# Kernel tuning notes

Measured on AMD Instinct MI355X. Metric: run time of the kernel, lower is better.

## Reference

```python
import jax, jax.numpy as jnp
import numpy as np

NEG_SLOPE = 0.2
N_NODES = 50000
N_EDGES = 800000
NUM_GRAPHS = 128
IN_F, HID_F, OUT_F = 64, 64, 64


def _gat_layer(x, src, dst, W, a_src, a_dst, b, n_nodes):
    # x: [N, Fin] -> out: [N, Fout]; single-head PyG GATConv with self-loops
    xp = x @ W                                   # [N, Fout]
    alpha_src = xp @ a_src                       # [N]
    alpha_dst = xp @ a_dst                       # [N]
    e = jax.nn.leaky_relu(alpha_src[src] + alpha_dst[dst], NEG_SLOPE)  # [E]
    # segment softmax over incoming edges of each dst node
    m = jax.ops.segment_max(e, dst, num_segments=n_nodes)
    ex = jnp.exp(e - m[dst])
    denom = jax.ops.segment_sum(ex, dst, num_segments=n_nodes)
    alpha = ex / denom[dst]                      # [E]
    out = jax.ops.segment_sum(alpha[:, None] * xp[src], dst, num_segments=n_nodes)
    return out + b


def setup_inputs() -> dict:
    key = jax.random.key(0)
    ks = jax.random.split(key, 12)
    x = jax.random.normal(ks[0], (N_NODES, IN_F), dtype=jnp.float32)
    edge_index = jax.random.randint(ks[1], (2, N_EDGES), 0, N_NODES, dtype=jnp.int64 if jax.config.jax_enable_x64 else jnp.int32)
    batch = jnp.sort(jax.random.randint(ks[2], (N_NODES,), 0, NUM_GRAPHS, dtype=edge_index.dtype))
    s = 0.1
    W1 = jax.random.normal(ks[3], (IN_F, HID_F), dtype=jnp.float32) * s
    att_src1 = jax.random.normal(ks[4], (HID_F,), dtype=jnp.float32) * s
    att_dst1 = jax.random.normal(ks[5], (HID_F,), dtype=jnp.float32) * s
    b1 = jax.random.normal(ks[6], (HID_F,), dtype=jnp.float32) * s
    W2 = jax.random.normal(ks[7], (HID_F, OUT_F), dtype=jnp.float32) * s
    att_src2 = jax.random.normal(ks[8], (OUT_F,), dtype=jnp.float32) * s
    att_dst2 = jax.random.normal(ks[9], (OUT_F,), dtype=jnp.float32) * s
    b2 = jax.random.normal(ks[10], (OUT_F,), dtype=jnp.float32) * s
    return {"x": x, "edge_index": edge_index, "batch": batch,
            "W1": W1, "att_src1": att_src1, "att_dst1": att_dst1, "b1": b1,
            "W2": W2, "att_src2": att_src2, "att_dst2": att_dst2, "b2": b2}


def reference(x, edge_index, batch, W1, att_src1, att_dst1, b1, W2, att_src2, att_dst2, b2):
    n = x.shape[0]
    # add self-loops (PyG GATConv default)
    loops = jnp.arange(n, dtype=edge_index.dtype)
    src = jnp.concatenate([edge_index[0], loops])
    dst = jnp.concatenate([edge_index[1], loops])
    h = _gat_layer(x, src, dst, W1, att_src1, att_dst1, b1, n)
    h = jax.nn.relu(h)  # dropout = identity at eval
    h = _gat_layer(h, src, dst, W2, att_src2, att_dst2, b2, n)
    h = jax.nn.relu(h)
    # scatter_mean over graphs
    sums = jax.ops.segment_sum(h, batch, num_segments=NUM_GRAPHS)
    counts = jax.ops.segment_sum(jnp.ones((n,), dtype=h.dtype), batch, num_segments=NUM_GRAPHS)
    return sums / jnp.maximum(counts, 1.0)[:, None]
```

## Files before the change

kernel.cpp:

```cpp
#include <hip/hip_runtime.h>
#include <hip/hip_fp16.h>

#define FEAT 64
#define BK   64
#define CAP  1536
#define MAXB 1024
#define SEPT 16
#define CHUNK (256 * SEPT)
#define LG   4

typedef _Float16 f16;
typedef __attribute__((ext_vector_type(8))) _Float16 f16x8;
typedef __attribute__((ext_vector_type(4))) float    f32x4;

struct GemmSm {
    union {
        struct { f16 Xs[64][72]; f16 Wt[64][72]; };
        float Cs[4][16][68];
    };
    float asl[64], adl[64];
};

__device__ __forceinline__ void gemm_tile(
    GemmSm& sm, int row0, const float* __restrict__ xin,
    const float* __restrict__ W, const float* __restrict__ avs,
    const float* __restrict__ avd, unsigned* __restrict__ xph,
    float* __restrict__ as_, float* __restrict__ ad_, int n)
{
    const int t = threadIdx.x;
    const int lane = t & 63;
    const int wave = t >> 6;

    if (t < 64) sm.asl[t] = avs[t];
    else if (t < 128) sm.adl[t - 64] = avd[t - 64];

    for (int i = t; i < 64 * 16; i += 256) {
        const int r = i >> 4, c4 = (i & 15) << 2;
        const int gr = row0 + r;
        float4 v = make_float4(0.f, 0.f, 0.f, 0.f);
        if (gr < n) v = *(const float4*)(xin + (size_t)gr * FEAT + c4);
        sm.Xs[r][c4 + 0] = (f16)v.x; sm.Xs[r][c4 + 1] = (f16)v.y;
        sm.Xs[r][c4 + 2] = (f16)v.z; sm.Xs[r][c4 + 3] = (f16)v.w;
    }
    for (int i = t; i < 64 * 16; i += 256) {
        const int k = i >> 4, c4 = (i & 15) << 2;
        const float4 v = *(const float4*)(W + k * FEAT + c4);
        sm.Wt[c4 + 0][k] = (f16)v.x; sm.Wt[c4 + 1][k] = (f16)v.y;
        sm.Wt[c4 + 2][k] = (f16)v.z; sm.Wt[c4 + 3][k] = (f16)v.w;
    }
    __syncthreads();

    const int mrow = (wave << 4) + (lane & 15);
    const int kg = lane >> 4;
    const f16x8 a0 = *(const f16x8*)(&sm.Xs[mrow][kg * 8]);
    const f16x8 a1 = *(const f16x8*)(&sm.Xs[mrow][32 + kg * 8]);

    f32x4 acc[4];
#pragma unroll
    for (int nt = 0; nt < 4; ++nt) {
        const int ncol = nt * 16 + (lane & 15);
        const f16x8 b0 = *(const f16x8*)(&sm.Wt[ncol][kg * 8]);
        const f16x8 b1 = *(const f16x8*)(&sm.Wt[ncol][32 + kg * 8]);
        f32x4 c = {0.f, 0.f, 0.f, 0.f};
        c = __builtin_amdgcn_mfma_f32_16x16x32_f16(a0, b0, c, 0, 0, 0);
        c = __builtin_amdgcn_mfma_f32_16x16x32_f16(a1, b1, c, 0, 0, 0);
        acc[nt] = c;
    }
    __syncthreads();

#pragma unroll
    for (int nt = 0; nt < 4; ++nt)
#pragma unroll
        for (int reg = 0; reg < 4; ++reg)
            sm.Cs[wave][(lane >> 4) * 4 + reg][nt * 16 + (lane & 15)] = acc[nt][reg];

    for (int i = lane; i < 16 * 32; i += 64) {
        const int r = i >> 5, fp = i & 31;
        const int node = row0 + (wave << 4) + r;
        if (node < n) {
            const __half2 pk = __floats2half2_rn(sm.Cs[wave][r][2 * fp],
                                                 sm.Cs[wave][r][2 * fp + 1]);
            xph[(size_t)node * 32 + fp] = *(const unsigned*)&pk;
        }
    }
    {
        const int r = lane >> 2, q = lane & 3;
        float s1 = 0.f, s2 = 0.f;
#pragma unroll
        for (int j = 0; j < 16; ++j) {
            const int c = q * 16 + j;
            const float v = sm.Cs[wave][r][c];
            s1 += v * sm.asl[c];
            s2 += v * sm.adl[c];
        }
        s1 += __shfl_xor(s1, 1); s1 += __shfl_xor(s1, 2);
        s2 += __shfl_xor(s2, 1); s2 += __shfl_xor(s2, 2);
        const int node = row0 + (wave << 4) + r;
        if (q == 0 && node < n) { as_[node] = s1; ad_[node] = s2; }
    }
}

__global__ __launch_bounds__(256) void scatter_gemm1_kernel(
    const int* __restrict__ src, const int* __restrict__ dst,
    int* __restrict__ bcur, unsigned* __restrict__ ebuf,
    const float* __restrict__ x, const float* __restrict__ W,
    const float* __restrict__ a_src, const float* __restrict__ a_dst,
    unsigned* __restrict__ xph, float* __restrict__ as_, float* __restrict__ ad_,
    int n, int E, int nbuck, int nchunks)
{
    __shared__ union {
        struct {
            unsigned staged[CHUNK];
            int hist[MAXB]; int lofs[MAXB]; int base[MAXB];
        } s;
        GemmSm g;
    } sm;

    const int t = threadIdx.x;
    const int lane = t & 63;
    const int wave = t >> 6;

    if (blockIdx.x < (unsigned)nchunks) {
        for (int i = t; i < nbuck; i += 256) sm.s.hist[i] = 0;
        __syncthreads();

        const int e0 = blockIdx.x * CHUNK;
        const int total = min(E - e0, CHUNK);

        unsigned code[SEPT]; int bk[SEPT], rk[SEPT];
#pragma unroll
        for (int k = 0; k < SEPT; ++k) {
            const int e = e0 + t + k * 256;
            bk[k] = -1;
            if (e < E) {
                const int s_ = src[e], d = dst[e];
                bk[k] = d >> 6;
                code[k] = ((unsigned)s_ << 6) | (unsigned)(d & 63);
                rk[k] = atomicAdd(&sm.s.hist[bk[k]], 1);
            }
        }
        __syncthreads();

        if (wave == 0) {
            int carry = 0;
            for (int b0 = 0; b0 < nbuck; b0 += 64) {
                const int idx = b0 + lane;
                int v = (idx < nbuck) ? sm.s.hist[idx] : 0;
                const int orig = v;
#pragma unroll
                for (int o = 1; o < 64; o <<= 1) {
                    const int u = __shfl_up(v, o);
                    if (lane >= o) v += u;
                }
                if (idx < nbuck) sm.s.lofs[idx] = v - orig + carry;
                carry += __shfl(v, 63);
            }
        }
        __syncthreads();
        for (int i = t; i < nbuck; i += 256) {
            const int hv = sm.s.hist[i];
            sm.s.base[i] = hv ? atomicAdd(&bcur[i], hv) : 0;
        }
        __syncthreads();

#pragma unroll
        for (int k = 0; k < SEPT; ++k) {
            if (bk[k] >= 0)
                sm.s.staged[sm.s.lofs[bk[k]] + rk[k]] =
                    ((unsigned)bk[k] << 22) | code[k];
        }
        __syncthreads();

        for (int i = t; i < total; i += 256) {
            const unsigned e = sm.s.staged[i];
            const int bkt = e >> 22;
            const int pos = sm.s.base[bkt] + (i - sm.s.lofs[bkt]);
            if (pos < CAP) ebuf[(size_t)bkt * CAP + pos] = e & 0x3FFFFFu;
        }
    } else {
        gemm_tile(sm.g, (blockIdx.x - nchunks) * 64, x, W, a_src, a_dst,
                  xph, as_, ad_, n);
    }
}

__device__ __forceinline__ void agg_phaseB_to(
    const unsigned* scode, const float* sw, const int* startsL,
    const float* adb, const float* __restrict__ as_,
    const uint4* __restrict__ xph4, const float* __restrict__ bias,
    float* __restrict__ hout, int hstride, int g0, int n)
{
    const int lane = threadIdx.x & 63;
    const int wave = threadIdx.x >> 6;
    const int np = lane >> 5;
    const int q  = (lane >> 3) & 3;
    const int fo = lane & 7;

    for (int pair = wave; pair < BK / 2; pair += 8) {
        const int node = pair * 2 + np;
        const int g = g0 + node;
        const int gc = (g < n) ? g : (n - 1);
        const int st = startsL[node], en = startsL[node + 1];

        float a[8] = {0.f, 0.f, 0.f, 0.f, 0.f, 0.f, 0.f, 0.f};
        float wsum = 0.f;

        int i = st + q;
        for (; i + 12 < en; i += 16) {
            const unsigned c0 = scode[i];
            const unsigned c1 = scode[i + 4];
            const unsigned c2 = scode[i + 8];
            const unsigned c3 = scode[i + 12];
            const float w0 = sw[i], w1 = sw[i + 4], w2 = sw[i + 8], w3 = sw[i + 12];
            const uint4 x0 = xph4[(size_t)(c0 >> 6) * 8 + fo];
            const uint4 x1 = xph4[(size_t)(c1 >> 6) * 8 + fo];
            const uint4 x2 = xph4[(size_t)(c2 >> 6) * 8 + fo];
            const uint4 x3 = xph4[(size_t)(c3 >> 6) * 8 + fo];
#pragma unroll
            for (int u = 0; u < 4; ++u) {
                const uint4 xv = (u == 0) ? x0 : (u == 1) ? x1 : (u == 2) ? x2 : x3;
                const float wv = (u == 0) ? w0 : (u == 1) ? w1 : (u == 2) ? w2 : w3;
                const __half2 p0 = *(const __half2*)&xv.x;
                const __half2 p1 = *(const __half2*)&xv.y;
                const __half2 p2 = *(const __half2*)&xv.z;
                const __half2 p3 = *(const __half2*)&xv.w;
                a[0] += wv * __low2float(p0);  a[1] += wv * __high2float(p0);
                a[2] += wv * __low2float(p1);  a[3] += wv * __high2float(p1);
                a[4] += wv * __low2float(p2);  a[5] += wv * __high2float(p2);
                a[6] += wv * __low2float(p3);  a[7] += wv * __high2float(p3);
            }
            wsum += (w0 + w1) + (w2 + w3);
        }
        for (; i < en; i += 4) {
            const unsigned c0 = scode[i];
            const float w0 = sw[i];
            const uint4 xv = xph4[(size_t)(c0 >> 6) * 8 + fo];
            const __half2 p0 = *(const __half2*)&xv.x;
            const __half2 p1 = *(const __half2*)&xv.y;
            const __half2 p2 = *(const __half2*)&xv.z;
            const __half2 p3 = *(const __half2*)&xv.w;
            a[0] += w0 * __low2float(p0);  a[1] += w0 * __high2float(p0);
            a[2] += w0 * __low2float(p1);  a[3] += w0 * __high2float(p1);
            a[4] += w0 * __low2float(p2);  a[5] += w0 * __high2float(p2);
            a[6] += w0 * __low2float(p3);  a[7] += w0 * __high2float(p3);
            wsum += w0;
        }

#pragma unroll
        for (int j = 0; j < 8; ++j) {
            a[j] += __shfl_xor(a[j], 8);
            a[j] += __shfl_xor(a[j], 16);
        }
        wsum += __shfl_xor(wsum, 8);
        wsum += __shfl_xor(wsum, 16);

        float tt = as_[gc] + adb[node];
        tt = (tt >= 0.f) ? tt : 0.2f * tt;
        const float wself = __expf(tt);
        const uint4 xg = xph4[(size_t)gc * 8 + fo];
        const __half2 s0 = *(const __half2*)&xg.x;
        const __half2 s1 = *(const __half2*)&xg.y;
        const __half2 s2 = *(const __half2*)&xg.z;
        const __half2 s3 = *(const __half2*)&xg.w;
        const float dinv = 1.f / (wsum + wself);
        const float4 bA = *(const float4*)(bias + 8 * fo);
        const float4 bB = *(const float4*)(bias + 8 * fo + 4);

        if (q == 0 && g < n) {
            float4 vA, vB;
            vA.x = fmaxf((a[0] + wself * __low2float(s0))  * dinv + bA.x, 0.f);
            vA.y = fmaxf((a[1] + wself * __high2float(s0)) * dinv + bA.y, 0.f);
            vA.z = fmaxf((a[2] + wself * __low2float(s1))  * dinv + bA.z, 0.f);
            vA.w = fmaxf((a[3] + wself * __high2float(s1)) * dinv + bA.w, 0.f);
            vB.x = fmaxf((a[4] + wself * __low2float(s2))  * dinv + bB.x, 0.f);
            vB.y = fmaxf((a[5] + wself * __high2float(s2)) * dinv + bB.y, 0.f);
            vB.z = fmaxf((a[6] + wself * __low2float(s3))  * dinv + bB.z, 0.f);
            vB.w = fmaxf((a[7] + wself * __high2float(s3)) * dinv + bB.w, 0.f);
            *(float4*)(hout + (size_t)node * hstride + 8 * fo)     = vA;
            *(float4*)(hout + (size_t)node * hstride + 8 * fo + 4) = vB;
        }
    }
}

__global__ __launch_bounds__(512) void sortagg1_gemm2_kernel(
    const int* __restrict__ bcur, unsigned* __restrict__ ebuf,
    int* __restrict__ startsG,
    const float* __restrict__ asA, const float* __restrict__ adA,
    const uint4* __restrict__ xphA, const float* __restrict__ b1,
    const float* __restrict__ W2, const float* __restrict__ asrc2,
    const float* __restrict__ adst2,
    unsigned* __restrict__ xphB, float* __restrict__ asB, float* __restrict__ adB,
    int n)
{
    __shared__ float htile[64][68];
    __shared__ union {
        struct { unsigned scode[CAP]; float sw[CAP]; int hist[BK]; int cur[BK]; } a;
        GemmSm g;
    } sm;
    __shared__ int starts[BK + 1];
    __shared__ float adb[BK];

    const int b = blockIdx.x;
    const int t = threadIdx.x;
    const int lane = t & 63, wave = t >> 6;
    const int g0 = b * BK;
    const int row0 = g0;

    if (t < BK) {
        sm.a.hist[t] = 0;
        adb[t] = (g0 + t < n) ? adA[g0 + t] : 0.f;
    }
    __syncthreads();

    int cnt = bcur[b];
    if (cnt > CAP) cnt = CAP;
    unsigned* eb = ebuf + (size_t)b * CAP;

    unsigned c[3];
#pragma unroll
    for (int k = 0; k < 3; ++k) {
        const int i = t + k * 512;
        if (i < cnt) { c[k] = eb[i]; atomicAdd(&sm.a.hist[c[k] & 63], 1); }
    }
    __syncthreads();
    if (wave == 0) {
        int v = sm.a.hist[lane];
#pragma unroll
        for (int o = 1; o < 64; o <<= 1) {
            const int u = __shfl_up(v, o);
            if (lane >= o) v += u;
        }
        starts[lane + 1] = v;
        sm.a.cur[lane] = v - sm.a.hist[lane];
        if (lane == 0) starts[0] = 0;
    }
    __syncthreads();
#pragma unroll
    for (int k = 0; k < 3; ++k) {
        const int i = t + k * 512;
        if (i < cnt) { const int p = atomicAdd(&sm.a.cur[c[k] & 63], 1); sm.a.scode[p] = c[k]; }
    }
    __syncthreads();

    unsigned cc[3]; float vv[3];
#pragma unroll
    for (int k = 0; k < 3; ++k) {
        const int i = t + k * 512;
        if (i < cnt) { cc[k] = sm.a.scode[i]; eb[i] = cc[k]; vv[k] = asA[cc[k] >> 6]; }
    }
    if (t <= BK) startsG[b * (BK + 1) + t] = starts[t];
#pragma unroll
    for (int k = 0; k < 3; ++k) {
        const int i = t + k * 512;
        if (i < cnt) {
            float tt = vv[k] + adb[cc[k] & 63];
            tt = (tt >= 0.f) ? tt : 0.2f * tt;
            sm.a.sw[i] = __expf(tt);
        }
    }
    __syncthreads();

    agg_phaseB_to(sm.a.scode, sm.a.sw, starts, adb, asA, xphA, b1,
                  &htile[0][0], 68, g0, n);
    __syncthreads();

    if (t < 64) sm.g.asl[t] = asrc2[t];
    else if (t < 128) sm.g.adl[t - 64] = adst2[t - 64];

    for (int i = t; i < 64 * 16; i += 512) {
        const int r = i >> 4, c4 = (i & 15) << 2;
        const float4 v = *(const float4*)(&htile[r][c4]);
        sm.g.Xs[r][c4 + 0] = (f16)v.x; sm.g.Xs[r][c4 + 1] = (f16)v.y;
        sm.g.Xs[r][c4 + 2] = (f16)v.z; sm.g.Xs[r][c4 + 3] = (f16)v.w;
    }
    for (int i = t; i < 64 * 16; i += 512) {
        const int k = i >> 4, c4 = (i & 15) << 2;
        const float4 v = *(const float4*)(W2 + k * FEAT + c4);
        sm.g.Wt[c4 + 0][k] = (f16)v.x; sm.g.Wt[c4 + 1][k] = (f16)v.y;
        sm.g.Wt[c4 + 2][k] = (f16)v.z; sm.g.Wt[c4 + 3][k] = (f16)v.w;
    }
    __syncthreads();

    f32x4 acc[4];
    if (wave < 4) {
        const int mrow = (wave << 4) + (lane & 15);
        const int kg = lane >> 4;
        const f16x8 a0 = *(const f16x8*)(&sm.g.Xs[mrow][kg * 8]);
        const f16x8 a1 = *(const f16x8*)(&sm.g.Xs[mrow][32 + kg * 8]);
#pragma unroll
        for (int nt = 0; nt < 4; ++nt) {
            const int ncol = nt * 16 + (lane & 15);
            const f16x8 b0 = *(const f16x8*)(&sm.g.Wt[ncol][kg * 8]);
            const f16x8 b1v = *(const f16x8*)(&sm.g.Wt[ncol][32 + kg * 8]);
            f32x4 cacc = {0.f, 0.f, 0.f, 0.f};
            cacc = __builtin_amdgcn_mfma_f32_16x16x32_f16(a0, b0, cacc, 0, 0, 0);
            cacc = __builtin_amdgcn_mfma_f32_16x16x32_f16(a1, b1v, cacc, 0, 0, 0);
            acc[nt] = cacc;
        }
    }
    __syncthreads();
    if (wave < 4) {
#pragma unroll
        for (int nt = 0; nt < 4; ++nt)
#pragma unroll
            for (int reg = 0; reg < 4; ++reg)
                sm.g.Cs[wave][(lane >> 4) * 4 + reg][nt * 16 + (lane & 15)] = acc[nt][reg];
    }
    __syncthreads();

    for (int i = t; i < 64 * 32; i += 512) {
        const int r = i >> 5, fp = i & 31;
        const int node = row0 + r;
        if (node < n) {
            const __half2 pk = __floats2half2_rn(sm.g.Cs[r >> 4][r & 15][2 * fp],
                                                 sm.g.Cs[r >> 4][r & 15][2 * fp + 1]);
            xphB[(size_t)node * 32 + fp] = *(const unsigned*)&pk;
        }
    }
    if (t < 256) {
        const int r = t >> 2, q = t & 3;
        float s1 = 0.f, s2 = 0.f;
#pragma unroll
        for (int j = 0; j < 16; ++j) {
            const int cidx = q * 16 + j;
            const float v = sm.g.Cs[r >> 4][r & 15][cidx];
            s1 += v * sm.g.asl[cidx];
            s2 += v * sm.g.adl[cidx];
        }
        s1 += __shfl_xor(s1, 1); s1 += __shfl_xor(s1, 2);
        s2 += __shfl_xor(s2, 1); s2 += __shfl_xor(s2, 2);
        const int node = row0 + r;
        if (q == 0 && node < n) { asB[node] = s1; adB[node] = s2; }
    }
}

__global__ __launch_bounds__(512) void agg2_pool_kernel(
    const unsigned* __restrict__ ebuf, const int* __restrict__ startsG,
    const float* __restrict__ as_, const float* __restrict__ ad_,
    const uint4* __restrict__ xph4, const float* __restrict__ bias,
    const int* __restrict__ batch, float* __restrict__ gpart,
    float* __restrict__ osum, int n)
{
    __shared__ unsigned scode[CAP];
    __shared__ float    sw[CAP];
    __shared__ int startsL[BK + 1];
    __shared__ float adb[BK];
    __shared__ int batchL[BK];
    __shared__ float gpartW[8][2][LG][FEAT];

    const int b = blockIdx.x;
    const int t = threadIdx.x;
    const int lane = t & 63, wave = t >> 6;
    const int g0 = b * BK;

    if (t < BK) {
        const int g = g0 + t;
        adb[t] = (g < n) ? ad_[g] : 0.f;
        batchL[t] = batch[(g < n) ? g : (n - 1)];
    }
    if (t <= BK) startsL[t] = startsG[b * (BK + 1) + t];
    for (int i = t; i < 8 * 2 * LG * FEAT; i += 512) ((float*)gpartW)[i] = 0.f;
    __syncthreads();

    const int cnt = startsL[BK];
    const unsigned* eb = ebuf + (size_t)b * CAP;

    unsigned cc[3]; float vv[3];
#pragma unroll
    for (int k = 0; k < 3; ++k) {
        const int i = t + k * 512;
        if (i < cnt) { cc[k] = eb[i]; vv[k] = as_[cc[k] >> 6]; }
    }
#pragma unroll
    for (int k = 0; k < 3; ++k) {
        const int i = t + k * 512;
        if (i < cnt) {
            float tt = vv[k] + adb[cc[k] & 63];
            tt = (tt >= 0.f) ? tt : 0.2f * tt;
            scode[i] = cc[k]; sw[i] = __expf(tt);
        }
    }
    __syncthreads();

    const int np = lane >> 5;
    const int q  = (lane >> 3) & 3;
    const int fo = lane & 7;
    const int gbase = batchL[0];

    for (int pair = wave; pair < BK / 2; pair += 8) {
        const int node = pair * 2 + np;
        const int g = g0 + node;
        const int gc = (g < n) ? g : (n - 1);
        const int st = startsL[node], en = startsL[node + 1];

        float a[8] = {0.f, 0.f, 0.f, 0.f, 0.f, 0.f, 0.f, 0.f};
        float wsum = 0.f;

        int i = st + q;
        for (; i + 12 < en; i += 16) {
            const unsigned c0 = scode[i];
            const unsigned c1 = scode[i + 4];
            const unsigned c2 = scode[i + 8];
            const unsigned c3 = scode[i + 12];
            const float w0 = sw[i], w1 = sw[i + 4], w2 = sw[i + 8], w3 = sw[i + 12];
            const uint4 x0 = xph4[(size_t)(c0 >> 6) * 8 + fo];
            const uint4 x1 = xph4[(size_t)(c1 >> 6) * 8 + fo];
            const uint4 x2 = xph4[(size_t)(c2 >> 6) * 8 + fo];
            const uint4 x3 = xph4[(size_t)(c3 >> 6) * 8 + fo];
#pragma unroll
            for (int u = 0; u < 4; ++u) {
                const uint4 xv = (u == 0) ? x0 : (u == 1) ? x1 : (u == 2) ? x2 : x3;
                const float wv = (u == 0) ? w0 : (u == 1) ? w1 : (u == 2) ? w2 : w3;
                const __half2 p0 = *(const __half2*)&xv.x;
                const __half2 p1 = *(const __half2*)&xv.y;
                const __half2 p2 = *(const __half2*)&xv.z;
                const __half2 p3 = *(const __half2*)&xv.w;
                a[0] += wv * __low2float(p0);  a[1] += wv * __high2float(p0);
                a[2] += wv * __low2float(p1);  a[3] += wv * __high2float(p1);
                a[4] += wv * __low2float(p2);  a[5] += wv * __high2float(p2);
                a[6] += wv * __low2float(p3);  a[7] += wv * __high2float(p3);
            }
            wsum += (w0 + w1) + (w2 + w3);
        }
        for (; i < en; i += 4) {
            const unsigned c0 = scode[i];
            const float w0 = sw[i];
            const uint4 xv = xph4[(size_t)(c0 >> 6) * 8 + fo];
            const __half2 p0 = *(const __half2*)&xv.x;
            const __half2 p1 = *(const __half2*)&xv.y;
            const __half2 p2 = *(const __half2*)&xv.z;
            const __half2 p3 = *(const __half2*)&xv.w;
            a[0] += w0 * __low2float(p0);  a[1] += w0 * __high2float(p0);
            a[2] += w0 * __low2float(p1);  a[3] += w0 * __high2float(p1);
            a[4] += w0 * __low2float(p2);  a[5] += w0 * __high2float(p2);
            a[6] += w0 * __low2float(p3);  a[7] += w0 * __high2float(p3);
            wsum += w0;
        }

#pragma unroll
        for (int j = 0; j < 8; ++j) {
            a[j] += __shfl_xor(a[j], 8);
            a[j] += __shfl_xor(a[j], 16);
        }
        wsum += __shfl_xor(wsum, 8);
        wsum += __shfl_xor(wsum, 16);

        float tt = as_[gc] + adb[node];
        tt = (tt >= 0.f) ? tt : 0.2f * tt;
        const float wself = __expf(tt);
        const uint4 xg = xph4[(size_t)gc * 8 + fo];
        const __half2 s0 = *(const __half2*)&xg.x;
        const __half2 s1 = *(const __half2*)&xg.y;
        const __half2 s2 = *(const __half2*)&xg.z;
        const __half2 s3 = *(const __half2*)&xg.w;
        const float dinv = 1.f / (wsum + wself);
        const float4 bA = *(const float4*)(bias + 8 * fo);
        const float4 bB = *(const float4*)(bias + 8 * fo + 4);

        if (q == 0 && g < n) {
            float4 vA, vB;
            vA.x = fmaxf((a[0] + wself * __low2float(s0))  * dinv + bA.x, 0.f);
            vA.y = fmaxf((a[1] + wself * __high2float(s0)) * dinv + bA.y, 0.f);
            vA.z = fmaxf((a[2] + wself * __low2float(s1))  * dinv + bA.z, 0.f);
            vA.w = fmaxf((a[3] + wself * __high2float(s1)) * dinv + bA.w, 0.f);
            vB.x = fmaxf((a[4] + wself * __low2float(s2))  * dinv + bB.x, 0.f);
            vB.y = fmaxf((a[5] + wself * __high2float(s2)) * dinv + bB.y, 0.f);
            vB.z = fmaxf((a[6] + wself * __low2float(s3))  * dinv + bB.z, 0.f);
            vB.w = fmaxf((a[7] + wself * __high2float(s3)) * dinv + bB.w, 0.f);

            const int lg = batchL[node] - gbase;
            if (lg < LG) {
                float* p = &gpartW[wave][np][lg][8 * fo];
                float4 oA = *(float4*)p;
                float4 oB = *(float4*)(p + 4);
                oA.x += vA.x; oA.y += vA.y; oA.z += vA.z; oA.w += vA.w;
                oB.x += vB.x; oB.y += vB.y; oB.z += vB.z; oB.w += vB.w;
                *(float4*)p = oA;
                *(float4*)(p + 4) = oB;
            } else {
                float* o = osum + (size_t)batchL[node] * FEAT + 8 * fo;
                atomicAdd(o + 0, vA.x); atomicAdd(o + 1, vA.y);
                atomicAdd(o + 2, vA.z); atomicAdd(o + 3, vA.w);
                atomicAdd(o + 4, vB.x); atomicAdd(o + 5, vB.y);
                atomicAdd(o + 6, vB.z); atomicAdd(o + 7, vB.w);
            }
        }
    }
    __syncthreads();

    if (t < LG * FEAT) {
        const int lg = t >> 6, f = t & 63;
        float s = 0.f;
#pragma unroll
        for (int w = 0; w < 8; ++w)
            s += gpartW[w][0][lg][f] + gpartW[w][1][lg][f];
        gpart[((size_t)b * LG + lg) * FEAT + f] = s;
    }
}

__device__ __forceinline__ int lower_bound_i(const int* a, int n, int key)
{
    int lo = 0, hi = n;
    while (lo < hi) {
        const int mid = (lo + hi) >> 1;
        if (a[mid] < key) lo = mid + 1; else hi = mid;
    }
    return lo;
}

__global__ __launch_bounds__(64) void pool_reduce_kernel(
    const float* __restrict__ gpart, const float* __restrict__ osum,
    const int* __restrict__ batch, float* __restrict__ out, int n, int G)
{
    const int g = blockIdx.x;
    const int lane = threadIdx.x;

    const int lo = lower_bound_i(batch, n, g);
    const int hi = lower_bound_i(batch, n, g + 1);

    float s = osum[(size_t)g * FEAT + lane];
    if (lo < hi) {
        const int b0 = lo >> 6, b1 = (hi - 1) >> 6;
        for (int b = b0; b <= b1; ++b) {
            const int base = batch[b << 6];
            const int lg = g - base;
            if (lg >= 0 && lg < LG)
                s += gpart[((size_t)b * LG + lg) * FEAT + lane];
        }
    }
    out[(size_t)g * FEAT + lane] = s / fmaxf((float)(hi - lo), 1.f);
}

extern "C" void kernel_launch(void* const* d_in, const int* in_sizes, int n_in,
                              void* d_out, int out_size, void* d_ws, size_t ws_size,
                              hipStream_t stream)
{
    const float* x      = (const float*)d_in[0];
    const int*   ei     = (const int*)d_in[1];
    const int*   batch  = (const int*)d_in[2];
    const float* W1     = (const float*)d_in[3];
    const float* asrc1  = (const float*)d_in[4];
    const float* adst1  = (const float*)d_in[5];
    const float* b1     = (const float*)d_in[6];
    const float* W2     = (const float*)d_in[7];
    const float* asrc2  = (const float*)d_in[8];
    const float* adst2  = (const float*)d_in[9];
    const float* b2     = (const float*)d_in[10];

    const int N = in_sizes[2];
    const int E = in_sizes[1] / 2;
    const int G = out_size / FEAT;

    const int* src = ei;
    const int* dst = ei + E;

    const int nbuck   = (N + BK - 1) / BK;
    const int nchunks = (E + CHUNK - 1) / CHUNK;
    const int gemmBlocks = (N + 63) / 64;

    unsigned* xphA    = (unsigned*)d_ws;
    unsigned* xphB    = xphA + (size_t)N * 32;
    float*    asA     = (float*)(xphB + (size_t)N * 32);
    float*    adA     = asA + N;
    float*    asB     = adA + N;
    float*    adB     = asB + N;
    int*      bcur    = (int*)(adB + N);
    float*    osum    = (float*)(bcur + nbuck);
    unsigned* ebuf    = (unsigned*)(osum + (size_t)G * FEAT);
    int*      startsG = (int*)(ebuf + (size_t)nbuck * CAP);
    float*    gpart   = (float*)(startsG + nbuck * (BK + 1));

    hipMemsetAsync(bcur, 0,
                   (size_t)nbuck * sizeof(int) + (size_t)G * FEAT * sizeof(float),
                   stream);
    scatter_gemm1_kernel<<<nchunks + gemmBlocks, 256, 0, stream>>>(
        src, dst, bcur, ebuf, x, W1, asrc1, adst1, xphA, asA, adA,
        N, E, nbuck, nchunks);
    sortagg1_gemm2_kernel<<<nbuck, 512, 0, stream>>>(
        bcur, ebuf, startsG, asA, adA, (const uint4*)xphA, b1,
        W2, asrc2, adst2, xphB, asB, adB, N);
    agg2_pool_kernel<<<nbuck, 512, 0, stream>>>(
        ebuf, startsG, asB, adB, (const uint4*)xphB, b2,
        batch, gpart, osum, N);
    pool_reduce_kernel<<<G, 64, 0, stream>>>(gpart, osum, batch,
                                             (float*)d_out, N, G);
}
```

Measured before the change: 175.5 us.

## Split layer-1 aggregation from GEMM2 and pool graph partials via atomics

Splits the fused sort/aggregate/GEMM2 kernel into a lighter aggregation kernel that writes fp16 hidden features to a global buffer, plus a separate MFMA GEMM2 kernel. This frees the shared memory held by the fused GEMM tile, so more blocks can run per CU, and adds min-occupancy launch bounds. Per-block pooled partials are now atomically added straight into the graph sums, which turns the final kernel into a simple normalise and drops the gpart scan. The cost is an extra launch, a round trip of the hidden features through global memory, and global atomics. LG shrinks from 4 to 2, which assumes a 64-node bucket never spans more than two graphs.

```diff
diff --git a/kernel.cpp b/kernel.cpp
--- a/kernel.cpp
+++ b/kernel.cpp
@@ -7,7 +7,7 @@
 #define MAXB 1024
 #define SEPT 16
 #define CHUNK (256 * SEPT)
-#define LG   4
+#define LG   2
 
 typedef _Float16 f16;
 typedef __attribute__((ext_vector_type(8))) _Float16 f16x8;
@@ -183,11 +183,11 @@
     }
 }
 
-__device__ __forceinline__ void agg_phaseB_to(
+__device__ __forceinline__ void agg_phaseB_hbuf(
     const unsigned* scode, const float* sw, const int* startsL,
     const float* adb, const float* __restrict__ as_,
     const uint4* __restrict__ xph4, const float* __restrict__ bias,
-    float* __restrict__ hout, int hstride, int g0, int n)
+    uint4* __restrict__ hbuf4, int g0, int n)
 {
     const int lane = threadIdx.x & 63;
     const int wave = threadIdx.x >> 6;
@@ -275,27 +275,30 @@
             vB.y = fmaxf((a[5] + wself * __high2float(s2)) * dinv + bB.y, 0.f);
             vB.z = fmaxf((a[6] + wself * __low2float(s3))  * dinv + bB.z, 0.f);
             vB.w = fmaxf((a[7] + wself * __high2float(s3)) * dinv + bB.w, 0.f);
-            *(float4*)(hout + (size_t)node * hstride + 8 * fo)     = vA;
-            *(float4*)(hout + (size_t)node * hstride + 8 * fo + 4) = vB;
-        }
-    }
-}
-
-__global__ __launch_bounds__(512) void sortagg1_gemm2_kernel(
+            const __half2 h01 = __floats2half2_rn(vA.x, vA.y);
+            const __half2 h23 = __floats2half2_rn(vA.z, vA.w);
+            const __half2 h45 = __floats2half2_rn(vB.x, vB.y);
+            const __half2 h67 = __floats2half2_rn(vB.z, vB.w);
+            uint4 pk;
+            pk.x = *(const unsigned*)&h01;
+            pk.y = *(const unsigned*)&h23;
+            pk.z = *(const unsigned*)&h45;
+            pk.w = *(const unsigned*)&h67;
+            hbuf4[(size_t)g * 8 + fo] = pk;
+        }
+    }
+}
+
+__global__ __launch_bounds__(512, 6) void sortagg1_kernel(
     const int* __restrict__ bcur, unsigned* __restrict__ ebuf,
     int* __restrict__ startsG,
     const float* __restrict__ asA, const float* __restrict__ adA,
     const uint4* __restrict__ xphA, const float* __restrict__ b1,
-    const float* __restrict__ W2, const float* __restrict__ asrc2,
-    const float* __restrict__ adst2,
-    unsigned* __restrict__ xphB, float* __restrict__ asB, float* __restrict__ adB,
-    int n)
-{
-    __shared__ float htile[64][68];
-    __shared__ union {
-        struct { unsigned scode[CAP]; float sw[CAP]; int hist[BK]; int cur[BK]; } a;
-        GemmSm g;
-    } sm;
+    uint4* __restrict__ hbuf4, int n)
+{
+    __shared__ unsigned scode[CAP];
+    __shared__ float    sw[CAP];
+    __shared__ int hist[BK], cur[BK];
     __shared__ int starts[BK + 1];
     __shared__ float adb[BK];
 
@@ -303,10 +306,9 @@
     const int t = threadIdx.x;
     const int lane = t & 63, wave = t >> 6;
     const int g0 = b * BK;
-    const int row0 = g0;
 
     if (t < BK) {
-        sm.a.hist[t] = 0;
+        hist[t] = 0;
         adb[t] = (g0 + t < n) ? adA[g0 + t] : 0.f;
     }
     __syncthreads();
@@ -319,25 +321,25 @@
 #pragma unroll
     for (int k = 0; k < 3; ++k) {
         const int i = t + k * 512;
-        if (i < cnt) { c[k] = eb[i]; atomicAdd(&sm.a.hist[c[k] & 63], 1); }
+        if (i < cnt) { c[k] = eb[i]; atomicAdd(&hist[c[k] & 63], 1); }
     }
     __syncthreads();
     if (wave == 0) {
-        int v = sm.a.hist[lane];
+        int v = hist[lane];
 #pragma unroll
         for (int o = 1; o < 64; o <<= 1) {
             const int u = __shfl_up(v, o);
             if (lane >= o) v += u;
         }
         starts[lane + 1] = v;
-        sm.a.cur[lane] = v - sm.a.hist[lane];
+        cur[lane] = v - hist[lane];
         if (lane == 0) starts[0] = 0;
     }
     __syncthreads();
 #pragma unroll
     for (int k = 0; k < 3; ++k) {
         const int i = t + k * 512;
-        if (i < cnt) { const int p = atomicAdd(&sm.a.cur[c[k] & 63], 1); sm.a.scode[p] = c[k]; }
+        if (i < cnt) { const int p = atomicAdd(&cur[c[k] & 63], 1); scode[p] = c[k]; }
     }
     __syncthreads();
 
@@ -345,7 +347,7 @@
 #pragma unroll
     for (int k = 0; k < 3; ++k) {
         const int i = t + k * 512;
-        if (i < cnt) { cc[k] = sm.a.scode[i]; eb[i] = cc[k]; vv[k] = asA[cc[k] >> 6]; }
+        if (i < cnt) { cc[k] = scode[i]; eb[i] = cc[k]; vv[k] = asA[cc[k] >> 6]; }
     }
     if (t <= BK) startsG[b * (BK + 1) + t] = starts[t];
 #pragma unroll
@@ -354,91 +356,99 @@
         if (i < cnt) {
             float tt = vv[k] + adb[cc[k] & 63];
             tt = (tt >= 0.f) ? tt : 0.2f * tt;
-            sm.a.sw[i] = __expf(tt);
-        }
-    }
-    __syncthreads();
-
-    agg_phaseB_to(sm.a.scode, sm.a.sw, starts, adb, asA, xphA, b1,
-                  &htile[0][0], 68, g0, n);
-    __syncthreads();
-
-    if (t < 64) sm.g.asl[t] = asrc2[t];
-    else if (t < 128) sm.g.adl[t - 64] = adst2[t - 64];
-
-    for (int i = t; i < 64 * 16; i += 512) {
-        const int r = i >> 4, c4 = (i & 15) << 2;
-        const float4 v = *(const float4*)(&htile[r][c4]);
-        sm.g.Xs[r][c4 + 0] = (f16)v.x; sm.g.Xs[r][c4 + 1] = (f16)v.y;
-        sm.g.Xs[r][c4 + 2] = (f16)v.z; sm.g.Xs[r][c4 + 3] = (f16)v.w;
-    }
-    for (int i = t; i < 64 * 16; i += 512) {
+            sw[i] = __expf(tt);
+        }
+    }
+    __syncthreads();
+
+    agg_phaseB_hbuf(scode, sw, starts, adb, asA, xphA, b1, hbuf4, g0, n);
+}
+
+__global__ __launch_bounds__(256) void gemm2_kernel(
+    const uint4* __restrict__ hbuf4,
+    const float* __restrict__ W, const float* __restrict__ avs,
+    const float* __restrict__ avd, unsigned* __restrict__ xph,
+    float* __restrict__ as_, float* __restrict__ ad_, int n)
+{
+    __shared__ GemmSm sm;
+    const int t = threadIdx.x;
+    const int lane = t & 63;
+    const int wave = t >> 6;
+    const int row0 = blockIdx.x * 64;
+
+    if (t < 64) sm.asl[t] = avs[t];
+    else if (t < 128) sm.adl[t - 64] = avd[t - 64];
+
+    for (int i = t; i < 64 * 8; i += 256) {
+        const int r = i >> 3, c = i & 7;
+        const int gr = row0 + r;
+        uint4 v = make_uint4(0u, 0u, 0u, 0u);
+        if (gr < n) v = hbuf4[(size_t)gr * 8 + c];
+        *(uint4*)(&sm.Xs[r][c * 8]) = v;
+    }
+    for (int i = t; i < 64 * 16; i += 256) {
         const int k = i >> 4, c4 = (i & 15) << 2;
-        const float4 v = *(const float4*)(W2 + k * FEAT + c4);
-        sm.g.Wt[c4 + 0][k] = (f16)v.x; sm.g.Wt[c4 + 1][k] = (f16)v.y;
-        sm.g.Wt[c4 + 2][k] = (f16)v.z; sm.g.Wt[c4 + 3][k] = (f16)v.w;
-    }
-    __syncthreads();
+        const float4 v = *(const float4*)(W + k * FEAT + c4);
+        sm.Wt[c4 + 0][k] = (f16)v.x; sm.Wt[c4 + 1][k] = (f16)v.y;
+        sm.Wt[c4 + 2][k] = (f16)v.z; sm.Wt[c4 + 3][k] = (f16)v.w;
+    }
+    __syncthreads();
+
+    const int mrow = (wave << 4) + (lane & 15);
+    const int kg = lane >> 4;
+    const f16x8 a0 = *(const f16x8*)(&sm.Xs[mrow][kg * 8]);
+    const f16x8 a1 = *(const f16x8*)(&sm.Xs[mrow][32 + kg * 8]);
 
     f32x4 acc[4];
-    if (wave < 4) {
-        const int mrow = (wave << 4) + (lane & 15);
-        const int kg = lane >> 4;
-        const f16x8 a0 = *(const f16x8*)(&sm.g.Xs[mrow][kg * 8]);
-        const f16x8 a1 = *(const f16x8*)(&sm.g.Xs[mrow][32 + kg * 8]);
-#pragma unroll
-        for (int nt = 0; nt < 4; ++nt) {
-            const int ncol = nt * 16 + (lane & 15);
-            const f16x8 b0 = *(const f16x8*)(&sm.g.Wt[ncol][kg * 8]);
-            const f16x8 b1v = *(const f16x8*)(&sm.g.Wt[ncol][32 + kg * 8]);
-            f32x4 cacc = {0.f, 0.f, 0.f, 0.f};
-            cacc = __builtin_amdgcn_mfma_f32_16x16x32_f16(a0, b0, cacc, 0, 0, 0);
-            cacc = __builtin_amdgcn_mfma_f32_16x16x32_f16(a1, b1v, cacc, 0, 0, 0);
-            acc[nt] = cacc;
-        }
-    }
-    __syncthreads();
-    if (wave < 4) {
-#pragma unroll
-        for (int nt = 0; nt < 4; ++nt)
-#pragma unroll
-            for (int reg = 0; reg < 4; ++reg)
-                sm.g.Cs[wave][(lane >> 4) * 4 + reg][nt * 16 + (lane & 15)] = acc[nt][reg];
-    }
-    __syncthreads();
-
-    for (int i = t; i < 64 * 32; i += 512) {
+#pragma unroll
+    for (int nt = 0; nt < 4; ++nt) {
+        const int ncol = nt * 16 + (lane & 15);
+        const f16x8 b0 = *(const f16x8*)(&sm.Wt[ncol][kg * 8]);
+        const f16x8 b1 = *(const f16x8*)(&sm.Wt[ncol][32 + kg * 8]);
+        f32x4 cv = {0.f, 0.f, 0.f, 0.f};
+        cv = __builtin_amdgcn_mfma_f32_16x16x32_f16(a0, b0, cv, 0, 0, 0);
+        cv = __builtin_amdgcn_mfma_f32_16x16x32_f16(a1, b1, cv, 0, 0, 0);
+        acc[nt] = cv;
+    }
+    __syncthreads();
+
+#pragma unroll
+    for (int nt = 0; nt < 4; ++nt)
+#pragma unroll
+        for (int reg = 0; reg < 4; ++reg)
+            sm.Cs[wave][(lane >> 4) * 4 + reg][nt * 16 + (lane & 15)] = acc[nt][reg];
+
+    for (int i = lane; i < 16 * 32; i += 64) {
         const int r = i >> 5, fp = i & 31;
-        const int node = row0 + r;
+        const int node = row0 + (wave << 4) + r;
         if (node < n) {
-            const __half2 pk = __floats2half2_rn(sm.g.Cs[r >> 4][r & 15][2 * fp],
-                                                 sm.g.Cs[r >> 4][r & 15][2 * fp + 1]);
-            xphB[(size_t)node * 32 + fp] = *(const unsigned*)&pk;
-        }
-    }
-    if (t < 256) {
-        const int r = t >> 2, q = t & 3;
+            const __half2 pk = __floats2half2_rn(sm.Cs[wave][r][2 * fp],
+                                                 sm.Cs[wave][r][2 * fp + 1]);
+            xph[(size_t)node * 32 + fp] = *(const unsigned*)&pk;
+        }
+    }
+    {
+        const int r = lane >> 2, q = lane & 3;
         float s1 = 0.f, s2 = 0.f;
 #pragma unroll
         for (int j = 0; j < 16; ++j) {
             const int cidx = q * 16 + j;
-            const float v = sm.g.Cs[r >> 4][r & 15][cidx];
-            s1 += v * sm.g.asl[cidx];
-            s2 += v * sm.g.adl[cidx];
+            const float v = sm.Cs[wave][r][cidx];
+            s1 += v * sm.asl[cidx];
+            s2 += v * sm.adl[cidx];
         }
         s1 += __shfl_xor(s1, 1); s1 += __shfl_xor(s1, 2);
         s2 += __shfl_xor(s2, 1); s2 += __shfl_xor(s2, 2);
-        const int node = row0 + r;
-        if (q == 0 && node < n) { asB[node] = s1; adB[node] = s2; }
-    }
-}
-
-__global__ __launch_bounds__(512) void agg2_pool_kernel(
+        const int node = row0 + (wave << 4) + r;
+        if (q == 0 && node < n) { as_[node] = s1; ad_[node] = s2; }
+    }
+}
+
+__global__ __launch_bounds__(512, 6) void agg2_pool_kernel(
     const unsigned* __restrict__ ebuf, const int* __restrict__ startsG,
     const float* __restrict__ as_, const float* __restrict__ ad_,
     const uint4* __restrict__ xph4, const float* __restrict__ bias,
-    const int* __restrict__ batch, float* __restrict__ gpart,
-    float* __restrict__ osum, int n)
+    const int* __restrict__ batch, float* __restrict__ osum, int n, int G)
 {
     __shared__ unsigned scode[CAP];
     __shared__ float    sw[CAP];
@@ -593,7 +603,9 @@
 #pragma unroll
         for (int w = 0; w < 8; ++w)
             s += gpartW[w][0][lg][f] + gpartW[w][1][lg][f];
-        gpart[((size_t)b * LG + lg) * FEAT + f] = s;
+        const int gg = batchL[0] + lg;
+        if (s != 0.f && gg < G)
+            atomicAdd(&osum[(size_t)gg * FEAT + f], s);
     }
 }
 
@@ -607,27 +619,16 @@
     return lo;
 }
 
-__global__ __launch_bounds__(64) void pool_reduce_kernel(
-    const float* __restrict__ gpart, const float* __restrict__ osum,
-    const int* __restrict__ batch, float* __restrict__ out, int n, int G)
+__global__ __launch_bounds__(64) void pool_norm_kernel(
+    const float* __restrict__ osum, const int* __restrict__ batch,
+    float* __restrict__ out, int n, int G)
 {
     const int g = blockIdx.x;
     const int lane = threadIdx.x;
-
     const int lo = lower_bound_i(batch, n, g);
     const int hi = lower_bound_i(batch, n, g + 1);
-
-    float s = osum[(size_t)g * FEAT + lane];
-    if (lo < hi) {
-        const int b0 = lo >> 6, b1 = (hi - 1) >> 6;
-        for (int b = b0; b <= b1; ++b) {
-            const int base = batch[b << 6];
-            const int lg = g - base;
-            if (lg >= 0 && lg < LG)
-                s += gpart[((size_t)b * LG + lg) * FEAT + lane];
-        }
-    }
-    out[(size_t)g * FEAT + lane] = s / fmaxf((float)(hi - lo), 1.f);
+    out[(size_t)g * FEAT + lane] =
+        osum[(size_t)g * FEAT + lane] / fmaxf((float)(hi - lo), 1.f);
 }
 
 extern "C" void kernel_launch(void* const* d_in, const int* in_sizes, int n_in,
@@ -667,7 +668,7 @@
     float*    osum    = (float*)(bcur + nbuck);
     unsigned* ebuf    = (unsigned*)(osum + (size_t)G * FEAT);
     int*      startsG = (int*)(ebuf + (size_t)nbuck * CAP);
-    float*    gpart   = (float*)(startsG + nbuck * (BK + 1));
+    unsigned* hbuf    = (unsigned*)(startsG + nbuck * (BK + 1));
 
     hipMemsetAsync(bcur, 0,
                    (size_t)nbuck * sizeof(int) + (size_t)G * FEAT * sizeof(float),
@@ -675,12 +676,13 @@
     scatter_gemm1_kernel<<<nchunks + gemmBlocks, 256, 0, stream>>>(
         src, dst, bcur, ebuf, x, W1, asrc1, adst1, xphA, asA, adA,
         N, E, nbuck, nchunks);
-    sortagg1_gemm2_kernel<<<nbuck, 512, 0, stream>>>(
+    sortagg1_kernel<<<nbuck, 512, 0, stream>>>(
         bcur, ebuf, startsG, asA, adA, (const uint4*)xphA, b1,
-        W2, asrc2, adst2, xphB, asB, adB, N);
+        (uint4*)hbuf, N);
+    gemm2_kernel<<<gemmBlocks, 256, 0, stream>>>(
+        (const uint4*)hbuf, W2, asrc2, adst2, xphB, asB, adB, N);
     agg2_pool_kernel<<<nbuck, 512, 0, stream>>>(
         ebuf, startsG, asB, adB, (const uint4*)xphB, b2,
-        batch, gpart, osum, N);
-    pool_reduce_kernel<<<G, 64, 0, stream>>>(gpart, osum, batch,
-                                             (float*)d_out, N, G);
-}
+        batch, osum, N, G);
+    pool_norm_kernel<<<G, 64, 0, stream>>>(osum, batch, (float*)d_out, N, G);
+}
```

Result: no change. 178.5 us (+1.8%).
